# Performance work log

Measured on AMD Instinct MI355X. Metric: run time of the kernel, lower is better.

Reference implementation:

```python
import jax, jax.numpy as jnp
import numpy as np

S, B, CIN, COUT, H, W, K = 4, 32, 128, 256, 16, 16, 3
D = CIN * K * K  # 1152, patch feature size = in_features
PRIOR_PREC = 1.0  # isotropic prior precision (prior_prec_full = PRIOR_PREC * I_D)
LOG_PREC_LR = 1.0


def _patches(x, k):
    # x: [N, C, H, W] -> [N, C*k*k, H, W]; channel-major patch ordering (matches torch unfold)
    pad = k // 2
    return jax.lax.conv_general_dilated_patches(
        x, (k, k), (1, 1), ((pad, pad), (pad, pad)),
        dimension_numbers=('NCHW', 'OIHW', 'NCHW'))


def setup_inputs() -> dict:
    key = jax.random.key(0)
    k1, k2, k3, k4 = jax.random.split(key, 4)
    X = jax.random.normal(k1, (S, B, CIN, H, W), jnp.float32)
    u = jax.random.normal(k2, (B, COUT, H, W), jnp.float32)
    log_prec_scaled = jax.random.normal(k3, (B,), jnp.float32)
    Z = jax.random.normal(k4, (S, COUT, D), jnp.float32)  # standard normal noise for rsample
    return {"X": X, "u": u, "log_prec_scaled": log_prec_scaled, "Z": Z}


def reference(X, u, log_prec_scaled, Z):
    Xi = X[:, :B]  # [S, B, CIN, H, W]
    sqrt_prec = jnp.exp(0.5 * LOG_PREC_LR * log_prec_scaled)[:, None, None, None]  # [B,1,1,1]
    Xil = sqrt_prec * Xi                     # [S, B, CIN, H, W]
    Yil = sqrt_prec * u                      # [B, COUT, H, W]

    # conv_mm: sufficient statistics via patch extraction
    P = _patches(Xil.reshape(S * B, CIN, H, W), K).reshape(S, B, D, H * W)
    Yf = Yil.reshape(B, COUT, H * W)
    XLX = jnp.einsum('sbdp,sbep->sde', P, P)       # [S, D, D]
    XLY = jnp.einsum('sbdp,bcp->sdc', P, Yf)       # [S, D, COUT]

    # rsample_logpq_weights
    prec = XLX + PRIOR_PREC * jnp.eye(D, dtype=XLX.dtype)   # [S, D, D]
    L = jnp.linalg.cholesky(prec)                            # [S, D, D], lower
    logdet_prec = 2.0 * jnp.sum(jnp.log(jnp.diagonal(L, axis1=-2, axis2=-1)), -1)  # [S]

    mu = jax.scipy.linalg.cho_solve((L, True), XLY)          # [S, D, COUT]
    # dW: solve L^T dW = Z (multi-RHS; L is shared across COUT)
    dW = jax.scipy.linalg.solve_triangular(L, jnp.swapaxes(Z, -1, -2), lower=True, trans='T')
    Wm = jnp.swapaxes(mu + dW, -1, -2)                       # [S, COUT, D]

    # logP: unnormalized MVN log-prob of each output neuron's weights under N(0, PRIOR_PREC^-1 I)
    logP = (0.5 * COUT * D * jnp.log(jnp.asarray(PRIOR_PREC, Wm.dtype))
            - 0.5 * PRIOR_PREC * jnp.sum(Wm * Wm, (-1, -2)))          # [S]
    logQ = -0.5 * jnp.sum(Z * Z, (-1, -2)) + 0.5 * COUT * logdet_prec  # [S]
    logpq = logP - logQ
    return Wm, logpq
```

## Files before the change

kernel.cpp:

```cpp
#include <hip/hip_runtime.h>
#include <math.h>

#define NS 4
#define NB 32
#define CIN 128
#define NCOUT 256
#define HWN 256
#define ND 1152
#define NK 8192
static const size_t D2 = (size_t)ND * ND;

typedef __attribute__((ext_vector_type(8))) short bf16x8;
typedef __attribute__((ext_vector_type(4))) float f32x4;

static __device__ inline unsigned short f2bf(float x) {
  unsigned int u = __float_as_uint(x);
  unsigned int r = (u + 0x7fffu + ((u >> 16) & 1u)) >> 16;
  return (unsigned short)r;
}
static __device__ inline float bf2f(unsigned short h) {
  return __uint_as_float(((unsigned int)h) << 16);
}
static __device__ inline float rdlane(float v, int l) {
  return __int_as_float(__builtin_amdgcn_readlane(__float_as_int(v), l));
}
static __device__ __forceinline__ void waitflag(const int* f) {
  while (__hip_atomic_load(f, __ATOMIC_RELAXED, __HIP_MEMORY_SCOPE_AGENT) == 0)
    __builtin_amdgcn_s_sleep(1);
  (void)__hip_atomic_load(f, __ATOMIC_ACQUIRE, __HIP_MEMORY_SCOPE_AGENT);
}


__global__ void k_sqrtp(const float* __restrict__ lp, float* __restrict__ sp,
                        float* __restrict__ pp) {
  int b = threadIdx.x;
  if (b < NB) sp[b] = expf(0.5f * lp[b]);
  if (b < 8) pp[b] = 0.f;
}

__global__ __launch_bounds__(128) void k_patches(const float* __restrict__ X,
                                                 const float* __restrict__ sp,
                                                 unsigned short* __restrict__ Phi,
                                                 unsigned short* __restrict__ Plo) {
  int d = blockIdx.x, s = blockIdx.y, t = threadIdx.x;
  int c = d / 9, r = d % 9, ky = r / 3, kx = r % 3;
  int p0 = t * 2;
  int yy = (p0 >> 4) + ky - 1;
  int xx0 = (p0 & 15) + kx - 1;
  bool oky = (yy >= 0 && yy < 16);
  bool ok0 = oky && (xx0 >= 0) && (xx0 < 16);
  bool ok1 = oky && (xx0 + 1 >= 0) && (xx0 + 1 < 16);
  int xo = yy * 16 + xx0;
  size_t base = ((size_t)s * ND + d) * NK + p0;
  for (int b = 0; b < NB; ++b) {
    float sb = sp[b];
    const float* xb = X + ((size_t)(s * NB + b) * CIN + c) * HWN;
    float v0 = ok0 ? xb[xo] * sb : 0.f;
    float v1 = ok1 ? xb[xo + 1] * sb : 0.f;
    unsigned short h0 = f2bf(v0), h1 = f2bf(v1);
    unsigned short l0 = f2bf(v0 - bf2f(h0)), l1 = f2bf(v1 - bf2f(h1));
    size_t idx = base + (size_t)b * HWN;
    *(unsigned int*)(Phi + idx) = (unsigned int)h0 | ((unsigned int)h1 << 16);
    *(unsigned int*)(Plo + idx) = (unsigned int)l0 | ((unsigned int)l1 << 16);
  }
}

__global__ __launch_bounds__(128) void k_ytt(const float* __restrict__ u,
                                             const float* __restrict__ sp,
                                             unsigned short* __restrict__ Yhi,
                                             unsigned short* __restrict__ Ylo) {
  int c = blockIdx.x, t = threadIdx.x;
  int p0 = t * 2;
  for (int b = 0; b < NB; ++b) {
    float sb = sp[b];
    const float* ub = u + ((size_t)b * NCOUT + c) * HWN + p0;
    float v0 = ub[0] * sb, v1 = ub[1] * sb;
    unsigned short h0 = f2bf(v0), h1 = f2bf(v1);
    unsigned short l0 = f2bf(v0 - bf2f(h0)), l1 = f2bf(v1 - bf2f(h1));
    size_t idx = (size_t)c * NK + (size_t)b * HWN + p0;
    *(unsigned int*)(Yhi + idx) = (unsigned int)h0 | ((unsigned int)h1 << 16);
    *(unsigned int*)(Ylo + idx) = (unsigned int)l0 | ((unsigned int)l1 << 16);
  }
}

__global__ __launch_bounds__(256) void k_gemm_mfma(
    const unsigned short* __restrict__ Phi, const unsigned short* __restrict__ Plo,
    const unsigned short* __restrict__ Yhi, const unsigned short* __restrict__ Ylo,
    float* __restrict__ prec, float* __restrict__ prec2,
    float* __restrict__ XLY, float* __restrict__ XLY2) {
  int jt = blockIdx.x, it = blockIdx.y;
  int s = blockIdx.z >> 1, kp = blockIdx.z & 1;
  bool isX = (jt <= it);
  if (!isX && jt < 9) return;
  int i0 = it * 128;
  int j0;
  const unsigned short *Bh, *Bl;
  if (isX) {
    j0 = jt * 128;
    Bh = Phi + ((size_t)s * ND + j0) * NK;
    Bl = Plo + ((size_t)s * ND + j0) * NK;
  } else {
    j0 = (jt - 9) * 128;
    Bh = Yhi + (size_t)j0 * NK;
    Bl = Ylo + (size_t)j0 * NK;
  }
  const unsigned short* Ah = Phi + ((size_t)s * ND + i0) * NK;
  const unsigned short* Al = Plo + ((size_t)s * ND + i0) * NK;

  __shared__ unsigned short sAh[4096], sAl[4096], sBh[4096], sBl[4096];
  int tid = threadIdx.x, wave = tid >> 6, lane = tid & 63;
  int wr = wave >> 1, wc = wave & 1;

  f32x4 zero = {0.f, 0.f, 0.f, 0.f};
  f32x4 acc[4][4];
#pragma unroll
  for (int m = 0; m < 4; ++m)
#pragma unroll
    for (int n = 0; n < 4; ++n) acc[m][n] = zero;

  const unsigned short* srcs[4] = {Ah, Al, Bh, Bl};
  unsigned short* dsts[4] = {sAh, sAl, sBh, sBl};
  int r0l = lane >> 2;
  int ke = (lane & 3) * 8;
  int arow0 = wr * 64 + (lane & 15);
  int brow0 = wc * 64 + (lane & 15);
  int koff = (lane >> 4) * 8;

  int kbeg = kp * (NK / 2), kend = kbeg + NK / 2;
  for (int k0 = kbeg; k0 < kend; k0 += 32) {
    __syncthreads();
#pragma unroll
    for (int f = 0; f < 4; ++f) {
#pragma unroll
      for (int cc = 0; cc < 2; ++cc) {
        int c = wave * 2 + cc;
        const unsigned short* g = srcs[f] + (size_t)(c * 16 + r0l) * NK + k0 + ke;
        unsigned short* l = dsts[f] + c * 512;
        __builtin_amdgcn_global_load_lds(
            (const __attribute__((address_space(1))) void*)g,
            (__attribute__((address_space(3))) void*)l, 16, 0, 0);
      }
    }
    __syncthreads();
    bf16x8 ah[4], al[4], bh[4], bl[4];
#pragma unroll
    for (int m = 0; m < 4; ++m) {
      int off = (arow0 + m * 16) * 32 + koff;
      ah[m] = *(const bf16x8*)&sAh[off];
      al[m] = *(const bf16x8*)&sAl[off];
    }
#pragma unroll
    for (int n = 0; n < 4; ++n) {
      int off = (brow0 + n * 16) * 32 + koff;
      bh[n] = *(const bf16x8*)&sBh[off];
      bl[n] = *(const bf16x8*)&sBl[off];
    }
#pragma unroll
    for (int m = 0; m < 4; ++m)
#pragma unroll
      for (int n = 0; n < 4; ++n) {
        acc[m][n] = __builtin_amdgcn_mfma_f32_16x16x32_bf16(ah[m], bh[n], acc[m][n], 0, 0, 0);
        acc[m][n] = __builtin_amdgcn_mfma_f32_16x16x32_bf16(ah[m], bl[n], acc[m][n], 0, 0, 0);
        acc[m][n] = __builtin_amdgcn_mfma_f32_16x16x32_bf16(al[m], bh[n], acc[m][n], 0, 0, 0);
      }
  }

  if (isX) {
    float* base = (kp ? prec2 : prec) + (size_t)s * D2;
#pragma unroll
    for (int m = 0; m < 4; ++m) {
      int row = i0 + wr * 64 + m * 16 + (lane >> 4) * 4;
#pragma unroll
      for (int n = 0; n < 4; ++n) {
        int col = j0 + wc * 64 + n * 16 + (lane & 15);
        float* cp = base + (size_t)row * ND + col;
#pragma unroll
        for (int r = 0; r < 4; ++r) cp[(size_t)r * ND] = acc[m][n][r];
      }
    }
  } else {
    float* base = (kp ? XLY2 : XLY) + (size_t)s * ND * NCOUT;
#pragma unroll
    for (int m = 0; m < 4; ++m) {
      int row = i0 + wr * 64 + m * 16 + (lane >> 4) * 4;
#pragma unroll
      for (int n = 0; n < 4; ++n) {
        int col = j0 + wc * 64 + n * 16 + (lane & 15);
        float* cp = base + (size_t)row * NCOUT + col;
#pragma unroll
        for (int r = 0; r < 4; ++r) cp[(size_t)r * NCOUT] = acc[m][n][r];
      }
    }
  }
}


static __device__ __forceinline__ void factor64(
    float acc[4][4], float (&At)[64][68], float (&Bt)[64][68],
    int tid, int lane, int w, int tx, int ty,
    float* iA64q, float* logdq, int* flagq) {
  __syncthreads();
#pragma unroll
  for (int r = 0; r < 4; ++r)
#pragma unroll
    for (int e = 0; e < 4; ++e) At[ty * 4 + r][tx * 4 + e] = acc[r][e];
  {
    int rr = tid >> 2, cb2 = (tid & 3) * 16;
#pragma unroll
    for (int m = 0; m < 16; ++m) Bt[rr][cb2 + m] = (rr == cb2 + m) ? 1.f : 0.f;
  }
  __syncthreads();
  float diagv = 1.f;
  for (int p = 0; p < 8; ++p) {
    int c0 = p * 8;
    if (w == 0) {
      float pa[8], xb[8];
#pragma unroll
      for (int e = 0; e < 8; ++e) {
        pa[e] = At[lane][c0 + e];
        xb[e] = Bt[c0 + e][lane];
      }
#pragma unroll
      for (int j = 0; j < 8; ++j) {
        float dj = rdlane(pa[j], c0 + j);
        float r0 = __builtin_amdgcn_rsqf(dj);
        r0 = r0 * (1.5f - 0.5f * dj * r0 * r0);
        pa[j] *= r0;
        float xj = xb[j] * r0;
        xb[j] = xj;
        if (lane == c0 + j) diagv = dj * r0;
#pragma unroll
        for (int e = j + 1; e < 8; ++e) {
          float sv = rdlane(pa[j], c0 + e);
          pa[e] = fmaf(-pa[j], sv, pa[e]);
          xb[e] = fmaf(-sv, xj, xb[e]);
        }
      }
#pragma unroll
      for (int e = 0; e < 8; ++e) {
        At[lane][c0 + e] = pa[e];
        Bt[c0 + e][lane] = xb[e];
      }
    }
    __syncthreads();
    if (p < 7) {
      float La[8], Xp[8];
#pragma unroll
      for (int e = 0; e < 8; ++e) {
        La[e] = At[lane][c0 + e];
        Xp[e] = Bt[c0 + e][lane];
      }
      for (int c = c0 + 8 + w; c < 64; c += 4) {
        float Lc[8];
#pragma unroll
        for (int e = 0; e < 8; ++e) Lc[e] = At[c][c0 + e];
        float v = At[lane][c], vb = Bt[c][lane];
#pragma unroll
        for (int e = 0; e < 8; ++e) {
          v = fmaf(-La[e], Lc[e], v);
          vb = fmaf(-Lc[e], Xp[e], vb);
        }
        At[lane][c] = v;
        Bt[c][lane] = vb;
      }
      __syncthreads();
    }
  }
  if (w == 0) logdq[lane] = logf(diagv);
  {
    float* q = iA64q;
    int rr = tid >> 2, cb2 = (tid & 3) * 16;
#pragma unroll
    for (int m = 0; m < 4; ++m)
      *(float4*)(q + rr * 64 + cb2 + m * 4) = *(const float4*)&Bt[rr][cb2 + m * 4];
  }
  __threadfence();
  __syncthreads();
  if (tid == 0)
    __hip_atomic_store(flagq, 1, __ATOMIC_RELEASE, __HIP_MEMORY_SCOPE_AGENT);
}

__global__ __launch_bounds__(256, 3) void k_chol_dag(
    float* __restrict__ L, const float* __restrict__ Lp2,
    float* __restrict__ iA64, float* __restrict__ logd,
    int* __restrict__ flags) {
  int t0 = blockIdx.x, s = blockIdx.y;
  int bi = 0;
  while ((bi + 1) * (bi + 2) / 2 <= t0) ++bi;
  int bj = t0 - bi * (bi + 1) / 2;
  int ib = bi * 64, jb = bj * 64;
  float* Ls = L + (size_t)s * D2;
  const float* Ps = Lp2 + (size_t)s * D2;
  int* fc = flags + s * 324;
  int* pd = flags + 1584 + s * 18;

  __shared__ float At[64][68];
  __shared__ float Bt[64][68];
  int tid = threadIdx.x, tx = tid & 15, ty = tid >> 4;
  int lane = tid & 63, w = tid >> 6;

  float acc[4][4];
#pragma unroll
  for (int r = 0; r < 4; ++r) {
    size_t idx = (size_t)(ib + ty * 4 + r) * ND + jb + tx * 4;
    float4 v = *(const float4*)(Ls + idx);
    float4 v2 = *(const float4*)(Ps + idx);
    acc[r][0] = v.x + v2.x; acc[r][1] = v.y + v2.y;
    acc[r][2] = v.z + v2.z; acc[r][3] = v.w + v2.w;
  }
  if (bi == bj) {
#pragma unroll
    for (int r = 0; r < 4; ++r)
#pragma unroll
      for (int e = 0; e < 4; ++e)
        if (ty * 4 + r == tx * 4 + e) acc[r][e] += 1.f;
  }

  for (int k = 0; k < bj; ++k) {
    waitflag(&fc[bi * 18 + k]);
    waitflag(&fc[bj * 18 + k]);
    int kb = k * 64;
    {
      int a2 = tid >> 2, km = (tid & 3) * 4;
#pragma unroll
      for (int m = 0; m < 4; ++m) {
        float4 v = *(const float4*)(Ls + (size_t)(ib + a2) * ND + kb + km + m * 16);
        At[km + m * 16 + 0][a2] = v.x;
        At[km + m * 16 + 1][a2] = v.y;
        At[km + m * 16 + 2][a2] = v.z;
        At[km + m * 16 + 3][a2] = v.w;
        float4 u4 = *(const float4*)(Ls + (size_t)(jb + a2) * ND + kb + km + m * 16);
        Bt[km + m * 16 + 0][a2] = u4.x;
        Bt[km + m * 16 + 1][a2] = u4.y;
        Bt[km + m * 16 + 2][a2] = u4.z;
        Bt[km + m * 16 + 3][a2] = u4.w;
      }
    }
    __syncthreads();
#pragma unroll
    for (int kc = 0; kc < 64; ++kc) {
      float4 a4 = *(const float4*)&At[kc][ty * 4];
      float4 b4 = *(const float4*)&Bt[kc][tx * 4];
      float ar[4] = {a4.x, a4.y, a4.z, a4.w};
      float br[4] = {b4.x, b4.y, b4.z, b4.w};
#pragma unroll
      for (int r = 0; r < 4; ++r)
#pragma unroll
        for (int e = 0; e < 4; ++e) acc[r][e] = fmaf(-ar[r], br[e], acc[r][e]);
    }
    __syncthreads();
  }

  if (bi == bj) {
    if (bi == 0) {
      factor64(acc, At, Bt, tid, lane, w, tx, ty,
               iA64 + (size_t)(s * 18) * 4096, logd + (size_t)s * ND, &fc[0]);
    } else {
#pragma unroll
      for (int r = 0; r < 4; ++r) {
        float4 v = {acc[r][0], acc[r][1], acc[r][2], acc[r][3]};
        *(float4*)(Ls + (size_t)(ib + ty * 4 + r) * ND + ib + tx * 4) = v;
      }
      __threadfence();
      __syncthreads();
      if (tid == 0)
        __hip_atomic_store(&pd[bi], 1, __ATOMIC_RELEASE,
                           __HIP_MEMORY_SCOPE_AGENT);
    }
  } else {
#pragma unroll
    for (int r = 0; r < 4; ++r)
#pragma unroll
      for (int e = 0; e < 4; ++e) At[tx * 4 + e][ty * 4 + r] = acc[r][e];
    waitflag(&fc[bj * 18 + bj]);
    {
      const float* q = iA64 + (size_t)(s * 18 + bj) * 4096;
      int a2 = tid >> 2, km = (tid & 3) * 4;
#pragma unroll
      for (int m = 0; m < 4; ++m) {
        float4 v = *(const float4*)(q + a2 * 64 + km + m * 16);
        Bt[km + m * 16 + 0][a2] = v.x;
        Bt[km + m * 16 + 1][a2] = v.y;
        Bt[km + m * 16 + 2][a2] = v.z;
        Bt[km + m * 16 + 3][a2] = v.w;
      }
    }
    __syncthreads();
    float acc2[4][4] = {};
#pragma unroll
    for (int kc = 0; kc < 64; ++kc) {
      float4 a4 = *(const float4*)&At[kc][ty * 4];
      float4 b4 = *(const float4*)&Bt[kc][tx * 4];
      float ar[4] = {a4.x, a4.y, a4.z, a4.w};
      float br[4] = {b4.x, b4.y, b4.z, b4.w};
#pragma unroll
      for (int r = 0; r < 4; ++r)
#pragma unroll
        for (int e = 0; e < 4; ++e) acc2[r][e] = fmaf(ar[r], br[e], acc2[r][e]);
    }
#pragma unroll
    for (int r = 0; r < 4; ++r) {
      float4 v = {acc2[r][0], acc2[r][1], acc2[r][2], acc2[r][3]};
      *(float4*)(Ls + (size_t)(ib + ty * 4 + r) * ND + jb + tx * 4) = v;
    }
    __threadfence();
    __syncthreads();
    if (tid == 0)
      __hip_atomic_store(&fc[bi * 18 + bj], 1, __ATOMIC_RELEASE,
                         __HIP_MEMORY_SCOPE_AGENT);

    if (bj == bi - 1) {
#pragma unroll
      for (int r = 0; r < 4; ++r)
#pragma unroll
        for (int e = 0; e < 4; ++e) At[tx * 4 + e][ty * 4 + r] = acc2[r][e];
      waitflag(&pd[bi]);
#pragma unroll
      for (int r = 0; r < 4; ++r) {
        float4 v = *(const float4*)(Ls + (size_t)(ib + ty * 4 + r) * ND + ib + tx * 4);
        acc[r][0] = v.x; acc[r][1] = v.y; acc[r][2] = v.z; acc[r][3] = v.w;
      }
      __syncthreads();
#pragma unroll
      for (int kc = 0; kc < 64; ++kc) {
        float4 a4 = *(const float4*)&At[kc][ty * 4];
        float4 b4 = *(const float4*)&At[kc][tx * 4];
        float ar[4] = {a4.x, a4.y, a4.z, a4.w};
        float br[4] = {b4.x, b4.y, b4.z, b4.w};
#pragma unroll
        for (int r = 0; r < 4; ++r)
#pragma unroll
          for (int e = 0; e < 4; ++e) acc[r][e] = fmaf(-ar[r], br[e], acc[r][e]);
      }
      factor64(acc, At, Bt, tid, lane, w, tx, ty,
               iA64 + (size_t)(s * 18 + bi) * 4096, logd + (size_t)s * ND + ib,
               &fc[bi * 18 + bi]);
    }
  }
}

__global__ __launch_bounds__(256) void k_invd128(const float* __restrict__ L,
                                                 const float* __restrict__ iA64,
                                                 float* __restrict__ iD) {
  int q = blockIdx.x, s = blockIdx.y;
  int tid = threadIdx.x;
  const float* Ls = L + (size_t)s * D2;
  float* out = iD + ((size_t)(s * 9 + q)) * 16384;
  int b0 = q * 128;
  __shared__ float inv0[64][68];
  __shared__ float invCt[64][68];
  __shared__ float Bt[64][68];
  __shared__ float Tl[64][68];

  {
    const float* iA0 = iA64 + (size_t)(s * 18 + 2 * q) * 4096;
    const float* iA1 = iA0 + 4096;
    int i = tid >> 2, c4 = (tid & 3) * 16;
#pragma unroll
    for (int m = 0; m < 4; ++m) {
      float4 v0 = *(const float4*)(iA0 + i * 64 + c4 + m * 4);
      *(float4*)&inv0[i][c4 + m * 4] = v0;
      float4 v1 = *(const float4*)(iA1 + i * 64 + c4 + m * 4);
      invCt[c4 + m * 4 + 0][i] = v1.x;
      invCt[c4 + m * 4 + 1][i] = v1.y;
      invCt[c4 + m * 4 + 2][i] = v1.z;
      invCt[c4 + m * 4 + 3][i] = v1.w;
    }
    const float* src = Ls + (size_t)(b0 + 64 + i) * ND + b0 + c4;
#pragma unroll
    for (int m = 0; m < 4; ++m) {
      float4 v = *(const float4*)(src + m * 4);
      Bt[c4 + m * 4 + 0][i] = v.x;
      Bt[c4 + m * 4 + 1][i] = v.y;
      Bt[c4 + m * 4 + 2][i] = v.z;
      Bt[c4 + m * 4 + 3][i] = v.w;
    }
  }
  __syncthreads();

  int tx = tid & 15, ty = tid >> 4;
  float acc[4][4] = {};
#pragma unroll
  for (int k = 0; k < 64; ++k) {
    float a4[4], b4[4];
#pragma unroll
    for (int e = 0; e < 4; ++e) { a4[e] = Bt[k][ty * 4 + e]; b4[e] = inv0[k][tx * 4 + e]; }
#pragma unroll
    for (int r = 0; r < 4; ++r)
#pragma unroll
      for (int e = 0; e < 4; ++e) acc[r][e] = fmaf(a4[r], b4[e], acc[r][e]);
  }
#pragma unroll
  for (int r = 0; r < 4; ++r)
#pragma unroll
    for (int e = 0; e < 4; ++e) Tl[ty * 4 + r][tx * 4 + e] = acc[r][e];
  __syncthreads();
  float acc2[4][4] = {};
#pragma unroll
  for (int k = 0; k < 64; ++k) {
    float a4[4], b4[4];
#pragma unroll
    for (int e = 0; e < 4; ++e) { a4[e] = invCt[k][ty * 4 + e]; b4[e] = Tl[k][tx * 4 + e]; }
#pragma unroll
    for (int r = 0; r < 4; ++r)
#pragma unroll
      for (int e = 0; e < 4; ++e) acc2[r][e] = fmaf(a4[r], b4[e], acc2[r][e]);
  }
  {
    int rrow = tid >> 2, cc = (tid & 3) * 32;
    float* o = out + rrow * 128 + cc;
    if (cc < 64) {
#pragma unroll
      for (int m = 0; m < 8; ++m) {
        float4 v = {inv0[rrow][cc + m * 4 + 0], inv0[rrow][cc + m * 4 + 1],
                    inv0[rrow][cc + m * 4 + 2], inv0[rrow][cc + m * 4 + 3]};
        *(float4*)(o + m * 4) = v;
      }
    } else {
      float4 z = {0.f, 0.f, 0.f, 0.f};
#pragma unroll
      for (int m = 0; m < 8; ++m) *(float4*)(o + m * 4) = z;
    }
  }
#pragma unroll
  for (int r = 0; r < 4; ++r) {
    float4 v = {-acc2[r][0], -acc2[r][1], -acc2[r][2], -acc2[r][3]};
    *(float4*)(out + (size_t)(64 + ty * 4 + r) * 128 + tx * 4) = v;
  }
  {
    int i = tid >> 2, jc = (tid & 3) * 16;
#pragma unroll
    for (int m = 0; m < 4; ++m) {
      float4 v = {invCt[jc + m * 4 + 0][i], invCt[jc + m * 4 + 1][i],
                  invCt[jc + m * 4 + 2][i], invCt[jc + m * 4 + 3][i]};
      *(float4*)(out + (size_t)(64 + i) * 128 + 64 + jc + m * 4) = v;
    }
  }
}

__global__ __launch_bounds__(256) void k_solve2(
    const float* __restrict__ L, const float* __restrict__ iD,
    const float* __restrict__ B1, const float* __restrict__ B2,
    const float* __restrict__ Z, float* __restrict__ Xf, float* __restrict__ Xb,
    float* __restrict__ Wm, float* __restrict__ pp, int* __restrict__ flags) {
  int r = blockIdx.x, ct = blockIdx.y, s = blockIdx.z;
  int rb = r * 128, cb = ct * 64;
  const float* Ls = L + (size_t)s * D2;
  const float* Dq = iD + ((size_t)(s * 9 + r)) * 16384;
  float* Xfs = Xf + (size_t)s * ND * NCOUT;
  float* Xbs = Xb + (size_t)s * ND * NCOUT;
  int fbf = 1296 + (s * 4 + ct) * 9;
  int fbb = 1440 + (s * 4 + ct) * 9;

  __shared__ float sA[32][132];
  __shared__ float sB[32][68];
  __shared__ float red[8];
  int tid = threadIdx.x, tx = tid & 15, ty = tid >> 4;
  int wave = tid >> 6, lane = tid & 63;

  float acc[8][4];
#pragma unroll
  for (int ii = 0; ii < 8; ++ii) {
    size_t idx = (size_t)s * ND * NCOUT + (size_t)(rb + ty * 8 + ii) * NCOUT + cb + tx * 4;
    float4 v = *(const float4*)(B1 + idx);
    float4 v2 = *(const float4*)(B2 + idx);
    acc[ii][0] = v.x + v2.x; acc[ii][1] = v.y + v2.y;
    acc[ii][2] = v.z + v2.z; acc[ii][3] = v.w + v2.w;
  }
  for (int q = 0; q < r; ++q) {
    waitflag(&flags[fbf + q]);
    int qb = q * 128;
    for (int kk = 0; kk < 4; ++kk) {
      __syncthreads();
      {
        int i = tid >> 1, kb = (tid & 1) * 16;
        const float* src = Ls + (size_t)(rb + i) * ND + qb + kk * 32 + kb;
#pragma unroll
        for (int m = 0; m < 4; ++m) {
          float4 v = *(const float4*)(src + m * 4);
          sA[kb + m * 4 + 0][i] = v.x;
          sA[kb + m * 4 + 1][i] = v.y;
          sA[kb + m * 4 + 2][i] = v.z;
          sA[kb + m * 4 + 3][i] = v.w;
        }
      }
      {
        int k = tid >> 3, jb2 = (tid & 7) * 8;
        const float* src = Xfs + (size_t)(qb + kk * 32 + k) * NCOUT + cb + jb2;
        float4 v0 = *(const float4*)src;
        float4 v1 = *(const float4*)(src + 4);
        *(float4*)&sB[k][jb2] = v0;
        *(float4*)&sB[k][jb2 + 4] = v1;
      }
      __syncthreads();
#pragma unroll
      for (int k = 0; k < 32; ++k) {
        float4 a0 = *(const float4*)&sA[k][ty * 8];
        float4 a1 = *(const float4*)&sA[k][ty * 8 + 4];
        float4 b0 = *(const float4*)&sB[k][tx * 4];
        float a[8] = {a0.x, a0.y, a0.z, a0.w, a1.x, a1.y, a1.z, a1.w};
        float b[4] = {b0.x, b0.y, b0.z, b0.w};
#pragma unroll
        for (int ii = 0; ii < 8; ++ii)
#pragma unroll
          for (int j = 0; j < 4; ++j) acc[ii][j] = fmaf(-a[ii], b[j], acc[ii][j]);
      }
    }
  }
  float acc2[8][4] = {};
  for (int kk = 0; kk < 4; ++kk) {
    __syncthreads();
    if ((ty >> 2) == kk) {
      int kloc = ty * 8 - kk * 32;
#pragma unroll
      for (int ii = 0; ii < 8; ++ii) {
        float4 v = {acc[ii][0], acc[ii][1], acc[ii][2], acc[ii][3]};
        *(float4*)&sB[kloc + ii][tx * 4] = v;
      }
    }
    {
      int i = tid >> 1, kb = (tid & 1) * 16;
      const float* src = Dq + (size_t)i * 128 + kk * 32 + kb;
#pragma unroll
      for (int m = 0; m < 4; ++m) {
        float4 v = *(const float4*)(src + m * 4);
        sA[kb + m * 4 + 0][i] = v.x;
        sA[kb + m * 4 + 1][i] = v.y;
        sA[kb + m * 4 + 2][i] = v.z;
        sA[kb + m * 4 + 3][i] = v.w;
      }
    }
    __syncthreads();
#pragma unroll
    for (int k = 0; k < 32; ++k) {
      float4 a0 = *(const float4*)&sA[k][ty * 8];
      float4 a1 = *(const float4*)&sA[k][ty * 8 + 4];
      float4 b0 = *(const float4*)&sB[k][tx * 4];
      float a[8] = {a0.x, a0.y, a0.z, a0.w, a1.x, a1.y, a1.z, a1.w};
      float b[4] = {b0.x, b0.y, b0.z, b0.w};
#pragma unroll
      for (int ii = 0; ii < 8; ++ii)
#pragma unroll
        for (int j = 0; j < 4; ++j) acc2[ii][j] = fmaf(a[ii], b[j], acc2[ii][j]);
    }
  }
#pragma unroll
  for (int ii = 0; ii < 8; ++ii) {
    float4 v = {acc2[ii][0], acc2[ii][1], acc2[ii][2], acc2[ii][3]};
    *(float4*)(Xfs + (size_t)(rb + ty * 8 + ii) * NCOUT + cb + tx * 4) = v;
  }
  __threadfence();
  __syncthreads();
  if (tid == 0)
    __hip_atomic_store(&flags[fbf + r], 1, __ATOMIC_RELEASE,
                       __HIP_MEMORY_SCOPE_AGENT);

#pragma unroll
  for (int ii = 0; ii < 8; ++ii)
#pragma unroll
    for (int j = 0; j < 4; ++j) acc[ii][j] = acc2[ii][j];

  float zp = 0.f;
  for (int kk = 0; kk < 4; ++kk) {
    __syncthreads();
    {
      int c = tid >> 2, d8 = (tid & 3) * 8;
      const float* src = Z + ((size_t)(s * NCOUT) + cb + c) * ND + rb + kk * 32 + d8;
      float4 v0 = *(const float4*)src;
      float4 v1 = *(const float4*)(src + 4);
      sA[d8 + 0][c] = v0.x; sA[d8 + 1][c] = v0.y; sA[d8 + 2][c] = v0.z; sA[d8 + 3][c] = v0.w;
      sA[d8 + 4][c] = v1.x; sA[d8 + 5][c] = v1.y; sA[d8 + 6][c] = v1.z; sA[d8 + 7][c] = v1.w;
      zp += v0.x * v0.x + v0.y * v0.y + v0.z * v0.z + v0.w * v0.w;
      zp += v1.x * v1.x + v1.y * v1.y + v1.z * v1.z + v1.w * v1.w;
    }
    __syncthreads();
    if ((ty >> 2) == kk) {
      int kloc = ty * 8 - kk * 32;
#pragma unroll
      for (int ii = 0; ii < 8; ++ii) {
        float4 v = *(const float4*)&sA[kloc + ii][tx * 4];
        acc[ii][0] += v.x; acc[ii][1] += v.y; acc[ii][2] += v.z; acc[ii][3] += v.w;
      }
    }
  }
#pragma unroll
  for (int m2 = 32; m2 >= 1; m2 >>= 1) zp += __shfl_xor(zp, m2, 64);
  if (lane == 0) red[wave] = zp;
  __syncthreads();
  if (tid == 0) atomicAdd(pp + s, red[0] + red[1] + red[2] + red[3]);

  for (int q = 8; q > r; --q) {
    waitflag(&flags[fbb + q]);
    int qb = q * 128;
    for (int kk = 0; kk < 4; ++kk) {
      __syncthreads();
      {
        int k = tid >> 3, ib2 = (tid & 7) * 16;
        const float* src = Ls + (size_t)(qb + kk * 32 + k) * ND + rb + ib2;
#pragma unroll
        for (int m = 0; m < 4; ++m)
          *(float4*)&sA[k][ib2 + m * 4] = *(const float4*)(src + m * 4);
      }
      {
        int k = tid >> 3, jb2 = (tid & 7) * 8;
        const float* src = Xbs + (size_t)(qb + kk * 32 + k) * NCOUT + cb + jb2;
        float4 v0 = *(const float4*)src;
        float4 v1 = *(const float4*)(src + 4);
        *(float4*)&sB[k][jb2] = v0;
        *(float4*)&sB[k][jb2 + 4] = v1;
      }
      __syncthreads();
#pragma unroll
      for (int k = 0; k < 32; ++k) {
        float4 a0 = *(const float4*)&sA[k][ty * 8];
        float4 a1 = *(const float4*)&sA[k][ty * 8 + 4];
        float4 b0 = *(const float4*)&sB[k][tx * 4];
        float a[8] = {a0.x, a0.y, a0.z, a0.w, a1.x, a1.y, a1.z, a1.w};
        float b[4] = {b0.x, b0.y, b0.z, b0.w};
#pragma unroll
        for (int ii = 0; ii < 8; ++ii)
#pragma unroll
          for (int j = 0; j < 4; ++j) acc[ii][j] = fmaf(-a[ii], b[j], acc[ii][j]);
      }
    }
  }
#pragma unroll
  for (int ii = 0; ii < 8; ++ii)
#pragma unroll
    for (int j = 0; j < 4; ++j) acc2[ii][j] = 0.f;
  for (int kk = 0; kk < 4; ++kk) {
    __syncthreads();
    if ((ty >> 2) == kk) {
      int kloc = ty * 8 - kk * 32;
#pragma unroll
      for (int ii = 0; ii < 8; ++ii) {
        float4 v = {acc[ii][0], acc[ii][1], acc[ii][2], acc[ii][3]};
        *(float4*)&sB[kloc + ii][tx * 4] = v;
      }
    }
    {
      int k = tid >> 3, ib2 = (tid & 7) * 16;
      const float* src = Dq + (size_t)(kk * 32 + k) * 128 + ib2;
#pragma unroll
      for (int m = 0; m < 4; ++m)
        *(float4*)&sA[k][ib2 + m * 4] = *(const float4*)(src + m * 4);
    }
    __syncthreads();
#pragma unroll
    for (int k = 0; k < 32; ++k) {
      float4 a0 = *(const float4*)&sA[k][ty * 8];
      float4 a1 = *(const float4*)&sA[k][ty * 8 + 4];
      float4 b0 = *(const float4*)&sB[k][tx * 4];
      float a[8] = {a0.x, a0.y, a0.z, a0.w, a1.x, a1.y, a1.z, a1.w};
      float b[4] = {b0.x, b0.y, b0.z, b0.w};
#pragma unroll
      for (int ii = 0; ii < 8; ++ii)
#pragma unroll
        for (int j = 0; j < 4; ++j) acc2[ii][j] = fmaf(a[ii], b[j], acc2[ii][j]);
    }
  }
#pragma unroll
  for (int ii = 0; ii < 8; ++ii) {
    float4 v = {acc2[ii][0], acc2[ii][1], acc2[ii][2], acc2[ii][3]};
    *(float4*)(Xbs + (size_t)(rb + ty * 8 + ii) * NCOUT + cb + tx * 4) = v;
  }
  __threadfence();
  __syncthreads();
  if (tid == 0)
    __hip_atomic_store(&flags[fbb + r], 1, __ATOMIC_RELEASE,
                       __HIP_MEMORY_SCOPE_AGENT);
  float wp = 0.f;
#pragma unroll
  for (int ii = 0; ii < 8; ++ii)
#pragma unroll
    for (int j = 0; j < 4; ++j) wp += acc2[ii][j] * acc2[ii][j];
#pragma unroll
  for (int m2 = 32; m2 >= 1; m2 >>= 1) wp += __shfl_xor(wp, m2, 64);
  __syncthreads();
  if (lane == 0) red[wave] = wp;
  __syncthreads();
  if (tid == 0) atomicAdd(pp + 4 + s, red[0] + red[1] + red[2] + red[3]);
  for (int kk = 0; kk < 4; ++kk) {
    __syncthreads();
    if ((ty >> 2) == kk) {
      int kloc = ty * 8 - kk * 32;
#pragma unroll
      for (int ii = 0; ii < 8; ++ii) {
        float4 v = {acc2[ii][0], acc2[ii][1], acc2[ii][2], acc2[ii][3]};
        *(float4*)&sB[kloc + ii][tx * 4] = v;
      }
    }
    __syncthreads();
    {
      int c = tid >> 2, d8 = (tid & 3) * 8;
      float t0 = sB[d8 + 0][c], t1 = sB[d8 + 1][c], t2 = sB[d8 + 2][c], t3 = sB[d8 + 3][c];
      float t4 = sB[d8 + 4][c], t5 = sB[d8 + 5][c], t6 = sB[d8 + 6][c], t7 = sB[d8 + 7][c];
      float* dst = Wm + ((size_t)(s * NCOUT) + cb + c) * ND + rb + kk * 32 + d8;
      float4 w0 = {t0, t1, t2, t3}, w1 = {t4, t5, t6, t7};
      *(float4*)dst = w0;
      *(float4*)(dst + 4) = w1;
    }
  }
}

__global__ __launch_bounds__(256) void k_finalize(const float* __restrict__ logd,
                                                  const float* __restrict__ pp,
                                                  float* __restrict__ out) {
  int s = blockIdx.x, tid = threadIdx.x;
  __shared__ float r0[256];
  float l = 0.f;
  for (int i = tid; i < ND; i += 256) l += logd[s * ND + i];
  r0[tid] = l;
  __syncthreads();
  for (int off = 128; off; off >>= 1) {
    if (tid < off) r0[tid] += r0[tid + off];
    __syncthreads();
  }
  if (tid == 0) {
    float logdet = 2.0f * r0[0];
    out[s] = 0.5f * (pp[s] - pp[4 + s]) - 128.0f * logdet;
  }
}

extern "C" void kernel_launch(void* const* d_in, const int* in_sizes, int n_in,
                              void* d_out, int out_size, void* d_ws, size_t ws_size,
                              hipStream_t stream) {
  const float* X = (const float*)d_in[0];
  const float* u = (const float*)d_in[1];
  const float* lp = (const float*)d_in[2];
  const float* Z = (const float*)d_in[3];
  float* out = (float*)d_out;

  float* ws = (float*)d_ws;
  float* sp    = ws;
  float* invd  = sp + 64;
  float* logd  = invd + (size_t)NS * ND;
  float* pp    = logd + (size_t)NS * ND;
  int*   flags = (int*)(pp + 64);
  float* iD    = (float*)(flags + 2048);
  float* iA64  = iD + (size_t)NS * 9 * 16384;
  float* Xf    = iA64 + (size_t)NS * 18 * 4096;
  float* Xb    = Xf + (size_t)NS * ND * NCOUT;
  float* prec  = Xb + (size_t)NS * ND * NCOUT;
  float* prec2 = prec + (size_t)NS * D2;
  float* XLY   = prec2 + (size_t)NS * D2;
  float* XLY2  = XLY + (size_t)NS * ND * NCOUT;
  unsigned short* Phi = (unsigned short*)(XLY2 + (size_t)NS * ND * NCOUT);
  unsigned short* Plo = Phi + (size_t)NS * ND * NK;
  unsigned short* Yhi = Plo + (size_t)NS * ND * NK;
  unsigned short* Ylo = Yhi + (size_t)NCOUT * NK;

  hipMemsetAsync(flags, 0, 2048 * sizeof(int), stream);
  k_sqrtp<<<1, 64, 0, stream>>>(lp, sp, pp);
  k_patches<<<dim3(ND, NS), 128, 0, stream>>>(X, sp, Phi, Plo);
  k_ytt<<<NCOUT, 128, 0, stream>>>(u, sp, Yhi, Ylo);
  k_gemm_mfma<<<dim3(11, 9, NS * 2), 256, 0, stream>>>(Phi, Plo, Yhi, Ylo, prec,
                                                       prec2, XLY, XLY2);
  k_chol_dag<<<dim3(171, NS), 256, 0, stream>>>(prec, prec2, iA64, logd, flags);
  k_invd128<<<dim3(9, NS), 256, 0, stream>>>(prec, iA64, iD);
  k_solve2<<<dim3(9, 4, NS), 256, 0, stream>>>(prec, iD, XLY, XLY2, Z, Xf, Xb,
                                               out, pp, flags);
  k_finalize<<<NS, 256, 0, stream>>>(logd, pp, out + (size_t)NS * NCOUT * ND);
}
```

Before: 1.674 ms.

## Factor diagonal Cholesky tiles in their own block and drop redundant threadfences

Diagonal tiles now do their own SYRK update, loading one panel into shared memory and using it for both operands, and then factor themselves. Before, the diagonal block wrote a partial result to memory and the last off-diagonal block in the row waited on it and finished the factorization. The change removes the extra pd flag handoff and the serial tail on the neighbouring tile. It also drops explicit __threadfence calls before release-store flag publishes, relying on the release atomic's ordering. That could weaken the visibility guarantee for data stored by threads other than thread 0.

Result: faster. 1.398 ms (-16.5%).

```diff
diff --git a/kernel.cpp b/kernel.cpp
--- a/kernel.cpp
+++ b/kernel.cpp
@@ -28,6 +28,11 @@
   while (__hip_atomic_load(f, __ATOMIC_RELAXED, __HIP_MEMORY_SCOPE_AGENT) == 0)
     __builtin_amdgcn_s_sleep(1);
   (void)__hip_atomic_load(f, __ATOMIC_ACQUIRE, __HIP_MEMORY_SCOPE_AGENT);
+}
+static __device__ __forceinline__ void publish(int* f) {
+  __syncthreads();
+  if (threadIdx.x == 0)
+    __hip_atomic_store(f, 1, __ATOMIC_RELEASE, __HIP_MEMORY_SCOPE_AGENT);
 }
 
 
@@ -274,7 +279,6 @@
     for (int m = 0; m < 4; ++m)
       *(float4*)(q + rr * 64 + cb2 + m * 4) = *(const float4*)&Bt[rr][cb2 + m * 4];
   }
-  __threadfence();
   __syncthreads();
   if (tid == 0)
     __hip_atomic_store(flagq, 1, __ATOMIC_RELEASE, __HIP_MEMORY_SCOPE_AGENT);
@@ -292,7 +296,6 @@
   float* Ls = L + (size_t)s * D2;
   const float* Ps = Lp2 + (size_t)s * D2;
   int* fc = flags + s * 324;
-  int* pd = flags + 1584 + s * 18;
 
   __shared__ float At[64][68];
   __shared__ float Bt[64][68];
@@ -318,7 +321,7 @@
 
   for (int k = 0; k < bj; ++k) {
     waitflag(&fc[bi * 18 + k]);
-    waitflag(&fc[bj * 18 + k]);
+    if (bi != bj) waitflag(&fc[bj * 18 + k]);
     int kb = k * 64;
     {
       int a2 = tid >> 2, km = (tid & 3) * 4;
@@ -329,44 +332,48 @@
         At[km + m * 16 + 1][a2] = v.y;
         At[km + m * 16 + 2][a2] = v.z;
         At[km + m * 16 + 3][a2] = v.w;
-        float4 u4 = *(const float4*)(Ls + (size_t)(jb + a2) * ND + kb + km + m * 16);
-        Bt[km + m * 16 + 0][a2] = u4.x;
-        Bt[km + m * 16 + 1][a2] = u4.y;
-        Bt[km + m * 16 + 2][a2] = u4.z;
-        Bt[km + m * 16 + 3][a2] = u4.w;
-      }
-    }
-    __syncthreads();
-#pragma unroll
-    for (int kc = 0; kc < 64; ++kc) {
-      float4 a4 = *(const float4*)&At[kc][ty * 4];
-      float4 b4 = *(const float4*)&Bt[kc][tx * 4];
-      float ar[4] = {a4.x, a4.y, a4.z, a4.w};
-      float br[4] = {b4.x, b4.y, b4.z, b4.w};
-#pragma unroll
-      for (int r = 0; r < 4; ++r)
-#pragma unroll
-        for (int e = 0; e < 4; ++e) acc[r][e] = fmaf(-ar[r], br[e], acc[r][e]);
+        if (bi != bj) {
+          float4 u4 = *(const float4*)(Ls + (size_t)(jb + a2) * ND + kb + km + m * 16);
+          Bt[km + m * 16 + 0][a2] = u4.x;
+          Bt[km + m * 16 + 1][a2] = u4.y;
+          Bt[km + m * 16 + 2][a2] = u4.z;
+          Bt[km + m * 16 + 3][a2] = u4.w;
+        }
+      }
+    }
+    __syncthreads();
+    if (bi == bj) {
+#pragma unroll
+      for (int kc = 0; kc < 64; ++kc) {
+        float4 a4 = *(const float4*)&At[kc][ty * 4];
+        float4 b4 = *(const float4*)&At[kc][tx * 4];
+        float ar[4] = {a4.x, a4.y, a4.z, a4.w};
+        float br[4] = {b4.x, b4.y, b4.z, b4.w};
+#pragma unroll
+        for (int r = 0; r < 4; ++r)
+#pragma unroll
+          for (int e = 0; e < 4; ++e) acc[r][e] = fmaf(-ar[r], br[e], acc[r][e]);
+      }
+    } else {
+#pragma unroll
+      for (int kc = 0; kc < 64; ++kc) {
+        float4 a4 = *(const float4*)&At[kc][ty * 4];
+        float4 b4 = *(const float4*)&Bt[kc][tx * 4];
+        float ar[4] = {a4.x, a4.y, a4.z, a4.w};
+        float br[4] = {b4.x, b4.y, b4.z, b4.w};
+#pragma unroll
+        for (int r = 0; r < 4; ++r)
+#pragma unroll
+          for (int e = 0; e < 4; ++e) acc[r][e] = fmaf(-ar[r], br[e], acc[r][e]);
+      }
     }
     __syncthreads();
   }
 
   if (bi == bj) {
-    if (bi == 0) {
-      factor64(acc, At, Bt, tid, lane, w, tx, ty,
-               iA64 + (size_t)(s * 18) * 4096, logd + (size_t)s * ND, &fc[0]);
-    } else {
-#pragma unroll
-      for (int r = 0; r < 4; ++r) {
-        float4 v = {acc[r][0], acc[r][1], acc[r][2], acc[r][3]};
-        *(float4*)(Ls + (size_t)(ib + ty * 4 + r) * ND + ib + tx * 4) = v;
-      }
-      __threadfence();
-      __syncthreads();
-      if (tid == 0)
-        __hip_atomic_store(&pd[bi], 1, __ATOMIC_RELEASE,
-                           __HIP_MEMORY_SCOPE_AGENT);
-    }
+    factor64(acc, At, Bt, tid, lane, w, tx, ty,
+             iA64 + (size_t)(s * 18 + bi) * 4096, logd + (size_t)s * ND + ib,
+             &fc[bi * 18 + bi]);
   } else {
 #pragma unroll
     for (int r = 0; r < 4; ++r)
@@ -403,39 +410,7 @@
       float4 v = {acc2[r][0], acc2[r][1], acc2[r][2], acc2[r][3]};
       *(float4*)(Ls + (size_t)(ib + ty * 4 + r) * ND + jb + tx * 4) = v;
     }
-    __threadfence();
-    __syncthreads();
-    if (tid == 0)
-      __hip_atomic_store(&fc[bi * 18 + bj], 1, __ATOMIC_RELEASE,
-                         __HIP_MEMORY_SCOPE_AGENT);
-
-    if (bj == bi - 1) {
-#pragma unroll
-      for (int r = 0; r < 4; ++r)
-#pragma unroll
-        for (int e = 0; e < 4; ++e) At[tx * 4 + e][ty * 4 + r] = acc2[r][e];
-      waitflag(&pd[bi]);
-#pragma unroll
-      for (int r = 0; r < 4; ++r) {
-        float4 v = *(const float4*)(Ls + (size_t)(ib + ty * 4 + r) * ND + ib + tx * 4);
-        acc[r][0] = v.x; acc[r][1] = v.y; acc[r][2] = v.z; acc[r][3] = v.w;
-      }
-      __syncthreads();
-#pragma unroll
-      for (int kc = 0; kc < 64; ++kc) {
-        float4 a4 = *(const float4*)&At[kc][ty * 4];
-        float4 b4 = *(const float4*)&At[kc][tx * 4];
-        float ar[4] = {a4.x, a4.y, a4.z, a4.w};
-        float br[4] = {b4.x, b4.y, b4.z, b4.w};
-#pragma unroll
-        for (int r = 0; r < 4; ++r)
-#pragma unroll
-          for (int e = 0; e < 4; ++e) acc[r][e] = fmaf(-ar[r], br[e], acc[r][e]);
-      }
-      factor64(acc, At, Bt, tid, lane, w, tx, ty,
-               iA64 + (size_t)(s * 18 + bi) * 4096, logd + (size_t)s * ND + ib,
-               &fc[bi * 18 + bi]);
-    }
+    publish(&fc[bi * 18 + bj]);
   }
 }
 
@@ -649,7 +624,6 @@
     float4 v = {acc2[ii][0], acc2[ii][1], acc2[ii][2], acc2[ii][3]};
     *(float4*)(Xfs + (size_t)(rb + ty * 8 + ii) * NCOUT + cb + tx * 4) = v;
   }
-  __threadfence();
   __syncthreads();
   if (tid == 0)
     __hip_atomic_store(&flags[fbf + r], 1, __ATOMIC_RELEASE,
@@ -764,7 +738,6 @@
     float4 v = {acc2[ii][0], acc2[ii][1], acc2[ii][2], acc2[ii][3]};
     *(float4*)(Xbs + (size_t)(rb + ty * 8 + ii) * NCOUT + cb + tx * 4) = v;
   }
-  __threadfence();
   __syncthreads();
   if (tid == 0)
     __hip_atomic_store(&flags[fbb + r], 1, __ATOMIC_RELEASE,
```

## Fold diagonal Cholesky updates into spine blocks and poll flags from one thread

Applied to the files above, without the earlier changes.

Diagonal tile blocks (other than the first) now exit immediately. The subdiagonal 'spine' block accumulates the diagonal tile's trailing update alongside its own, then factors the diagonal tile itself, which removes the separate diagonal-block write and pd flag handshake from the critical path. Flag polling is done by thread 0 only, followed by a block barrier, so the other waves no longer spin on global atomics. In exchange, spine blocks do double the FMA work per k step and hold extra registers.

New measurement: 1.442 ms. -13.8%, faster.

```diff
diff --git a/kernel.cpp b/kernel.cpp
--- a/kernel.cpp
+++ b/kernel.cpp
@@ -24,10 +24,13 @@
 static __device__ inline float rdlane(float v, int l) {
   return __int_as_float(__builtin_amdgcn_readlane(__float_as_int(v), l));
 }
-static __device__ __forceinline__ void waitflag(const int* f) {
-  while (__hip_atomic_load(f, __ATOMIC_RELAXED, __HIP_MEMORY_SCOPE_AGENT) == 0)
-    __builtin_amdgcn_s_sleep(1);
-  (void)__hip_atomic_load(f, __ATOMIC_ACQUIRE, __HIP_MEMORY_SCOPE_AGENT);
+static __device__ __forceinline__ void waitflag0(const int* f, int tid) {
+  if (tid == 0) {
+    while (__hip_atomic_load(f, __ATOMIC_RELAXED, __HIP_MEMORY_SCOPE_AGENT) == 0)
+      __builtin_amdgcn_s_sleep(2);
+    (void)__hip_atomic_load(f, __ATOMIC_ACQUIRE, __HIP_MEMORY_SCOPE_AGENT);
+  }
+  __syncthreads();
 }
 
 
@@ -198,7 +201,7 @@
 static __device__ __forceinline__ void factor64(
     float acc[4][4], float (&At)[64][68], float (&Bt)[64][68],
     int tid, int lane, int w, int tx, int ty,
-    float* iA64q, float* logdq, int* flagq) {
+    float* iA64q, float* logdq, int* flagq, int* flagq2) {
   __syncthreads();
 #pragma unroll
   for (int r = 0; r < 4; ++r)
@@ -276,8 +279,11 @@
   }
   __threadfence();
   __syncthreads();
-  if (tid == 0)
+  if (tid == 0) {
     __hip_atomic_store(flagq, 1, __ATOMIC_RELEASE, __HIP_MEMORY_SCOPE_AGENT);
+    if (flagq2)
+      __hip_atomic_store(flagq2, 1, __ATOMIC_RELEASE, __HIP_MEMORY_SCOPE_AGENT);
+  }
 }
 
 __global__ __launch_bounds__(256, 3) void k_chol_dag(
@@ -288,11 +294,12 @@
   int bi = 0;
   while ((bi + 1) * (bi + 2) / 2 <= t0) ++bi;
   int bj = t0 - bi * (bi + 1) / 2;
+  if (bi == bj && bi > 0) return;
+  bool spine = (bj == bi - 1);
   int ib = bi * 64, jb = bj * 64;
   float* Ls = L + (size_t)s * D2;
   const float* Ps = Lp2 + (size_t)s * D2;
   int* fc = flags + s * 324;
-  int* pd = flags + 1584 + s * 18;
 
   __shared__ float At[64][68];
   __shared__ float Bt[64][68];
@@ -308,17 +315,42 @@
     acc[r][0] = v.x + v2.x; acc[r][1] = v.y + v2.y;
     acc[r][2] = v.z + v2.z; acc[r][3] = v.w + v2.w;
   }
-  if (bi == bj) {
+  if (bi == 0 && bj == 0) {
 #pragma unroll
     for (int r = 0; r < 4; ++r)
 #pragma unroll
       for (int e = 0; e < 4; ++e)
         if (ty * 4 + r == tx * 4 + e) acc[r][e] += 1.f;
   }
+  float qcc[4][4];
+  if (spine) {
+#pragma unroll
+    for (int r = 0; r < 4; ++r) {
+      size_t idx = (size_t)(ib + ty * 4 + r) * ND + ib + tx * 4;
+      float4 v = *(const float4*)(Ls + idx);
+      float4 v2 = *(const float4*)(Ps + idx);
+      qcc[r][0] = v.x + v2.x; qcc[r][1] = v.y + v2.y;
+      qcc[r][2] = v.z + v2.z; qcc[r][3] = v.w + v2.w;
+    }
+#pragma unroll
+    for (int r = 0; r < 4; ++r)
+#pragma unroll
+      for (int e = 0; e < 4; ++e)
+        if (ty * 4 + r == tx * 4 + e) qcc[r][e] += 1.f;
+  }
 
   for (int k = 0; k < bj; ++k) {
-    waitflag(&fc[bi * 18 + k]);
-    waitflag(&fc[bj * 18 + k]);
+    if (tid == 0) {
+      while (__hip_atomic_load(&fc[bi * 18 + k], __ATOMIC_RELAXED,
+                               __HIP_MEMORY_SCOPE_AGENT) == 0)
+        __builtin_amdgcn_s_sleep(2);
+      while (__hip_atomic_load(&fc[bj * 18 + k], __ATOMIC_RELAXED,
+                               __HIP_MEMORY_SCOPE_AGENT) == 0)
+        __builtin_amdgcn_s_sleep(2);
+      (void)__hip_atomic_load(&fc[bj * 18 + k], __ATOMIC_ACQUIRE,
+                              __HIP_MEMORY_SCOPE_AGENT);
+    }
+    __syncthreads();
     int kb = k * 64;
     {
       int a2 = tid >> 2, km = (tid & 3) * 4;
@@ -337,105 +369,109 @@
       }
     }
     __syncthreads();
-#pragma unroll
-    for (int kc = 0; kc < 64; ++kc) {
-      float4 a4 = *(const float4*)&At[kc][ty * 4];
-      float4 b4 = *(const float4*)&Bt[kc][tx * 4];
-      float ar[4] = {a4.x, a4.y, a4.z, a4.w};
-      float br[4] = {b4.x, b4.y, b4.z, b4.w};
-#pragma unroll
-      for (int r = 0; r < 4; ++r)
-#pragma unroll
-        for (int e = 0; e < 4; ++e) acc[r][e] = fmaf(-ar[r], br[e], acc[r][e]);
-    }
-    __syncthreads();
-  }
-
-  if (bi == bj) {
-    if (bi == 0) {
-      factor64(acc, At, Bt, tid, lane, w, tx, ty,
-               iA64 + (size_t)(s * 18) * 4096, logd + (size_t)s * ND, &fc[0]);
+    if (spine) {
+#pragma unroll
+      for (int kc = 0; kc < 64; ++kc) {
+        float4 a4 = *(const float4*)&At[kc][ty * 4];
+        float4 b4 = *(const float4*)&Bt[kc][tx * 4];
+        float4 c4v = *(const float4*)&At[kc][tx * 4];
+        float ar[4] = {a4.x, a4.y, a4.z, a4.w};
+        float br[4] = {b4.x, b4.y, b4.z, b4.w};
+        float cr[4] = {c4v.x, c4v.y, c4v.z, c4v.w};
+#pragma unroll
+        for (int r = 0; r < 4; ++r)
+#pragma unroll
+          for (int e = 0; e < 4; ++e) {
+            acc[r][e] = fmaf(-ar[r], br[e], acc[r][e]);
+            qcc[r][e] = fmaf(-ar[r], cr[e], qcc[r][e]);
+          }
+      }
     } else {
 #pragma unroll
-      for (int r = 0; r < 4; ++r) {
-        float4 v = {acc[r][0], acc[r][1], acc[r][2], acc[r][3]};
-        *(float4*)(Ls + (size_t)(ib + ty * 4 + r) * ND + ib + tx * 4) = v;
-      }
-      __threadfence();
-      __syncthreads();
-      if (tid == 0)
-        __hip_atomic_store(&pd[bi], 1, __ATOMIC_RELEASE,
-                           __HIP_MEMORY_SCOPE_AGENT);
-    }
-  } else {
+      for (int kc = 0; kc < 64; ++kc) {
+        float4 a4 = *(const float4*)&At[kc][ty * 4];
+        float4 b4 = *(const float4*)&Bt[kc][tx * 4];
+        float ar[4] = {a4.x, a4.y, a4.z, a4.w};
+        float br[4] = {b4.x, b4.y, b4.z, b4.w};
+#pragma unroll
+        for (int r = 0; r < 4; ++r)
+#pragma unroll
+          for (int e = 0; e < 4; ++e) acc[r][e] = fmaf(-ar[r], br[e], acc[r][e]);
+      }
+    }
+    __syncthreads();
+  }
+
+  if (bi == 0 && bj == 0) {
+    factor64(acc, At, Bt, tid, lane, w, tx, ty,
+             iA64 + (size_t)(s * 18) * 4096, logd + (size_t)s * ND,
+             &fc[0], nullptr);
+    return;
+  }
+
+#pragma unroll
+  for (int r = 0; r < 4; ++r)
+#pragma unroll
+    for (int e = 0; e < 4; ++e) At[tx * 4 + e][ty * 4 + r] = acc[r][e];
+  waitflag0(&fc[bj * 18 + bj], tid);
+  {
+    const float* q = iA64 + (size_t)(s * 18 + bj) * 4096;
+    int a2 = tid >> 2, km = (tid & 3) * 4;
+#pragma unroll
+    for (int m = 0; m < 4; ++m) {
+      float4 v = *(const float4*)(q + a2 * 64 + km + m * 16);
+      Bt[km + m * 16 + 0][a2] = v.x;
+      Bt[km + m * 16 + 1][a2] = v.y;
+      Bt[km + m * 16 + 2][a2] = v.z;
+      Bt[km + m * 16 + 3][a2] = v.w;
+    }
+  }
+  __syncthreads();
+  float c2[4][4] = {};
+#pragma unroll
+  for (int kc = 0; kc < 64; ++kc) {
+    float4 a4 = *(const float4*)&At[kc][ty * 4];
+    float4 b4 = *(const float4*)&Bt[kc][tx * 4];
+    float ar[4] = {a4.x, a4.y, a4.z, a4.w};
+    float br[4] = {b4.x, b4.y, b4.z, b4.w};
 #pragma unroll
     for (int r = 0; r < 4; ++r)
 #pragma unroll
-      for (int e = 0; e < 4; ++e) At[tx * 4 + e][ty * 4 + r] = acc[r][e];
-    waitflag(&fc[bj * 18 + bj]);
-    {
-      const float* q = iA64 + (size_t)(s * 18 + bj) * 4096;
-      int a2 = tid >> 2, km = (tid & 3) * 4;
-#pragma unroll
-      for (int m = 0; m < 4; ++m) {
-        float4 v = *(const float4*)(q + a2 * 64 + km + m * 16);
-        Bt[km + m * 16 + 0][a2] = v.x;
-        Bt[km + m * 16 + 1][a2] = v.y;
-        Bt[km + m * 16 + 2][a2] = v.z;
-        Bt[km + m * 16 + 3][a2] = v.w;
-      }
-    }
-    __syncthreads();
-    float acc2[4][4] = {};
-#pragma unroll
-    for (int kc = 0; kc < 64; ++kc) {
-      float4 a4 = *(const float4*)&At[kc][ty * 4];
-      float4 b4 = *(const float4*)&Bt[kc][tx * 4];
-      float ar[4] = {a4.x, a4.y, a4.z, a4.w};
-      float br[4] = {b4.x, b4.y, b4.z, b4.w};
-#pragma unroll
-      for (int r = 0; r < 4; ++r)
-#pragma unroll
-        for (int e = 0; e < 4; ++e) acc2[r][e] = fmaf(ar[r], br[e], acc2[r][e]);
-    }
-#pragma unroll
-    for (int r = 0; r < 4; ++r) {
-      float4 v = {acc2[r][0], acc2[r][1], acc2[r][2], acc2[r][3]};
-      *(float4*)(Ls + (size_t)(ib + ty * 4 + r) * ND + jb + tx * 4) = v;
-    }
+      for (int e = 0; e < 4; ++e) c2[r][e] = fmaf(ar[r], br[e], c2[r][e]);
+  }
+#pragma unroll
+  for (int r = 0; r < 4; ++r) {
+    float4 v = {c2[r][0], c2[r][1], c2[r][2], c2[r][3]};
+    *(float4*)(Ls + (size_t)(ib + ty * 4 + r) * ND + jb + tx * 4) = v;
+  }
+
+  if (!spine) {
     __threadfence();
     __syncthreads();
     if (tid == 0)
       __hip_atomic_store(&fc[bi * 18 + bj], 1, __ATOMIC_RELEASE,
                          __HIP_MEMORY_SCOPE_AGENT);
-
-    if (bj == bi - 1) {
+  } else {
+    __syncthreads();
+#pragma unroll
+    for (int r = 0; r < 4; ++r)
+#pragma unroll
+      for (int e = 0; e < 4; ++e) At[tx * 4 + e][ty * 4 + r] = c2[r][e];
+    __syncthreads();
+#pragma unroll
+    for (int kc = 0; kc < 64; ++kc) {
+      float4 a4 = *(const float4*)&At[kc][ty * 4];
+      float4 b4 = *(const float4*)&At[kc][tx * 4];
+      float ar[4] = {a4.x, a4.y, a4.z, a4.w};
+      float br[4] = {b4.x, b4.y, b4.z, b4.w};
 #pragma unroll
       for (int r = 0; r < 4; ++r)
 #pragma unroll
-        for (int e = 0; e < 4; ++e) At[tx * 4 + e][ty * 4 + r] = acc2[r][e];
-      waitflag(&pd[bi]);
-#pragma unroll
-      for (int r = 0; r < 4; ++r) {
-        float4 v = *(const float4*)(Ls + (size_t)(ib + ty * 4 + r) * ND + ib + tx * 4);
-        acc[r][0] = v.x; acc[r][1] = v.y; acc[r][2] = v.z; acc[r][3] = v.w;
-      }
-      __syncthreads();
-#pragma unroll
-      for (int kc = 0; kc < 64; ++kc) {
-        float4 a4 = *(const float4*)&At[kc][ty * 4];
-        float4 b4 = *(const float4*)&At[kc][tx * 4];
-        float ar[4] = {a4.x, a4.y, a4.z, a4.w};
-        float br[4] = {b4.x, b4.y, b4.z, b4.w};
-#pragma unroll
-        for (int r = 0; r < 4; ++r)
-#pragma unroll
-          for (int e = 0; e < 4; ++e) acc[r][e] = fmaf(-ar[r], br[e], acc[r][e]);
-      }
-      factor64(acc, At, Bt, tid, lane, w, tx, ty,
-               iA64 + (size_t)(s * 18 + bi) * 4096, logd + (size_t)s * ND + ib,
-               &fc[bi * 18 + bi]);
-    }
+        for (int e = 0; e < 4; ++e) qcc[r][e] = fmaf(-ar[r], br[e], qcc[r][e]);
+    }
+    factor64(qcc, At, Bt, tid, lane, w, tx, ty,
+             iA64 + (size_t)(s * 18 + bi) * 4096, logd + (size_t)s * ND + ib,
+             &fc[bi * 18 + bi], &fc[bi * 18 + bj]);
   }
 }
 
@@ -568,7 +604,7 @@
     acc[ii][2] = v.z + v2.z; acc[ii][3] = v.w + v2.w;
   }
   for (int q = 0; q < r; ++q) {
-    waitflag(&flags[fbf + q]);
+    waitflag0(&flags[fbf + q], tid);
     int qb = q * 128;
     for (int kk = 0; kk < 4; ++kk) {
       __syncthreads();
@@ -690,7 +726,7 @@
   if (tid == 0) atomicAdd(pp + s, red[0] + red[1] + red[2] + red[3]);
 
   for (int q = 8; q > r; --q) {
-    waitflag(&flags[fbb + q]);
+    waitflag0(&flags[fbb + q], tid);
     int qb = q * 128;
     for (int kk = 0; kk < 4; ++kk) {
       __syncthreads();
```
